# Kernel optimization log

Measured on AMD Instinct MI355X. Metric: run time of the kernel, lower is better.

The kernel has to match this reference:

```python
import jax, jax.numpy as jnp
import numpy as np

H = 8            # kv heads
R = 2            # qhead_ratio -> hq = 16 query heads
D = 128          # head_size
DEG = 2          # power degree
GATE_OFFSET = 6.906768  # ~log(999), gates start near 1


def setup_inputs() -> dict:
    key = jax.random.key(0)
    ks = jax.random.split(key, 7)
    B, T, C = 1, 2048, 2048
    q_dim = H * R * D   # 2048
    kv_dim = H * D      # 1024
    s = 0.02
    return {
        "hidden_states": jax.random.normal(ks[0], (B, T, C), dtype=jnp.float32),
        "Wq": jax.random.normal(ks[1], (C, q_dim), dtype=jnp.float32) * s,
        "Wk": jax.random.normal(ks[2], (C, kv_dim), dtype=jnp.float32) * s,
        "Wv": jax.random.normal(ks[3], (C, kv_dim), dtype=jnp.float32) * s,
        "Wg": jax.random.normal(ks[4], (C, H), dtype=jnp.float32) * s,
        "Wc": jax.random.normal(ks[5], (q_dim, C), dtype=jnp.float32) * s,
        "bc": jnp.zeros((C,), dtype=jnp.float32),
    }


def _power_attention(q, k, v, log_g):
    # q: [B,T,hq,D], k/v: [B,T,H,D], log_g: [B,T,H]
    B, T, hq, d = q.shape
    scale = 1.0 / d ** 0.5
    # GQA: query head i uses kv head i // R (q was viewed as (B,T,H,R,D))
    k = jnp.repeat(k, R, axis=2)            # [B,T,hq,D]
    v = jnp.repeat(v, R, axis=2)            # [B,T,hq,D]
    logG = jnp.cumsum(log_g, axis=1)        # [B,T,H]
    logG = jnp.repeat(logG, R, axis=2)      # [B,T,hq]
    logG = jnp.transpose(logG, (0, 2, 1))   # [B,hq,T]
    qk = jnp.einsum('bthd,bshd->bhts', q, k) * scale   # [B,hq,T,T]
    a = qk ** DEG                                       # even degree -> >= 0
    # gating decay exp(logG_t - logG_s) <= 1 for s <= t
    gate = logG[:, :, :, None] - logG[:, :, None, :]    # [B,hq,T,T]
    causal = jnp.tril(jnp.ones((T, T), dtype=bool))
    a = jnp.where(causal, a * jnp.exp(gate), 0.0)
    norm = jnp.sum(a, axis=-1) + 1e-6                   # [B,hq,T]
    y = jnp.einsum('bhts,bshd->bthd', a, v)             # [B,T,hq,D]
    y = y / jnp.transpose(norm, (0, 2, 1))[..., None]
    return y


def reference(hidden_states, Wq, Wk, Wv, Wg, Wc, bc):
    B, T, C = hidden_states.shape
    q = (hidden_states @ Wq).reshape(B, T, H * R, D)
    k = (hidden_states @ Wk).reshape(B, T, H, D)
    v = (hidden_states @ Wv).reshape(B, T, H, D)
    g = hidden_states @ Wg                              # [B,T,H]
    log_g = jax.nn.log_sigmoid(GATE_OFFSET + g.astype(jnp.float32))
    y = _power_attention(q, k, v, log_g)                # [B,T,hq,D]
    y = y.reshape(B, T, H * R * D)
    return y @ Wc + bc
```

## Files before the change

### kernel.cpp

```cpp
#include <hip/hip_runtime.h>

typedef unsigned short u16;
typedef unsigned int u32;
typedef unsigned long long u64;
typedef __bf16 bf16x8 __attribute__((ext_vector_type(8)));
typedef float f32x4 __attribute__((ext_vector_type(4)));

union FragAB {
  bf16x8 v;
  u16 u[8];
  u32 w[4];
  u64 d2[2];
};

__device__ __forceinline__ u16 f2bf(float f) {
  u32 u = __builtin_bit_cast(u32, f);
  u += 0x7fffu + ((u >> 16) & 1u);
  return (u16)(u >> 16);
}

__device__ __forceinline__ void gload_lds16(const void* g, void* l) {
  __builtin_amdgcn_global_load_lds((__attribute__((address_space(1))) void*)g,
                                   (__attribute__((address_space(3))) void*)l, 16, 0, 0);
}

__device__ __forceinline__ int permcol(int n) {
  int k = n & 31;
  return (n & ~31) | ((k & 12) << 1) | ((k & 16) >> 2) | (k & 3);
}

__global__ __launch_bounds__(256) void conv_perm_kernel(const float* __restrict__ in,
                                                        u16* __restrict__ out, int n4) {
  int i = blockIdx.x * 256 + threadIdx.x;
  if (i >= n4) return;
  float4 v = ((const float4*)in)[i];
  u64 pk = (u64)f2bf(v.x) | ((u64)f2bf(v.y) << 16) | ((u64)f2bf(v.z) << 32) |
           ((u64)f2bf(v.w) << 48);
  int col = (i << 2) & 2047;
  int g = (col >> 2) & 7;
  int ncol = (col & ~31) | ((2 * (g & 3) + (g >> 2)) << 2);
  size_t row = (size_t)(i >> 9);
  *(u64*)&out[row * 2048 + ncol] = pk;
}

__global__ __launch_bounds__(256) void tconv_kernel(const float* __restrict__ in,
                                                    u16* __restrict__ out, int K, int N) {
  __shared__ float tile[32][33];
  int col = threadIdx.x & 31;
  int row0 = threadIdx.x >> 5;
  int kb = blockIdx.y * 32, nb = blockIdx.x * 32;
  int pcol = permcol(col);
#pragma unroll
  for (int i = 0; i < 4; i++) {
    int r = row0 + i * 8;
    tile[r][col] = in[(size_t)(kb + r) * N + nb + col];
  }
  __syncthreads();
#pragma unroll
  for (int i = 0; i < 4; i++) {
    int r = row0 + i * 8;
    out[(size_t)(nb + r) * K + kb + pcol] = f2bf(tile[col][r]);
  }
}

__global__ __launch_bounds__(256) void tconv3_kernel(const float* __restrict__ Wq,
                                                     const float* __restrict__ Wk,
                                                     const float* __restrict__ Wv,
                                                     u16* __restrict__ slab) {
  __shared__ float tile[32][33];
  const int z = blockIdx.z;
  const float* src = (z < 2) ? Wq : (z == 2 ? Wk : Wv);
  const int srcN = (z < 2) ? 2048 : 1024;
  const int colBase = (z == 1) ? 1024 : 0;
  const int dstRowBase = z * 1024;
  int col = threadIdx.x & 31;
  int row0 = threadIdx.x >> 5;
  int kb = blockIdx.y * 32, nb = blockIdx.x * 32;
  int pcol = permcol(col);
#pragma unroll
  for (int i = 0; i < 4; i++) {
    int r = row0 + i * 8;
    tile[r][col] = src[(size_t)(kb + r) * srcN + colBase + nb + col];
  }
  __syncthreads();
#pragma unroll
  for (int i = 0; i < 4; i++) {
    int r = row0 + i * 8;
    slab[(size_t)(dstRowBase + nb + r) * 2048 + kb + pcol] = f2bf(tile[col][r]);
  }
}

__global__ __launch_bounds__(256) void gate_kernel(const float* __restrict__ hs,
                                                   const float* __restrict__ Wg,
                                                   float* __restrict__ lgt) {
  int lane = threadIdx.x & 63, wid = threadIdx.x >> 6;
  int t = blockIdx.x * 4 + wid;
  float acc[8] = {0.f, 0.f, 0.f, 0.f, 0.f, 0.f, 0.f, 0.f};
  for (int c = lane; c < 2048; c += 64) {
    float x = hs[(size_t)t * 2048 + c];
    float4 w0 = *(const float4*)&Wg[c * 8];
    float4 w1 = *(const float4*)&Wg[c * 8 + 4];
    acc[0] += x * w0.x; acc[1] += x * w0.y; acc[2] += x * w0.z; acc[3] += x * w0.w;
    acc[4] += x * w1.x; acc[5] += x * w1.y; acc[6] += x * w1.z; acc[7] += x * w1.w;
  }
#pragma unroll
  for (int h = 0; h < 8; h++) {
    float v = acc[h];
    for (int m = 1; m < 64; m <<= 1) v += __shfl_xor(v, m, 64);
    if (lane == 0) {
      float x = 6.906768f + v;
      lgt[h * 2048 + t] = -log1pf(__expf(-x));
    }
  }
}

__global__ __launch_bounds__(256) void cumsum_kernel(const float* __restrict__ lgt,
                                                     float* __restrict__ logG) {
  int h = blockIdx.x;
  __shared__ float buf[2048];
  for (int i = threadIdx.x; i < 2048; i += 256) buf[i] = lgt[h * 2048 + i];
  __syncthreads();
  for (int off = 1; off < 2048; off <<= 1) {
    float tmp[8];
#pragma unroll
    for (int j = 0; j < 8; j++) {
      int i = threadIdx.x + j * 256;
      tmp[j] = (i >= off) ? buf[i - off] : 0.f;
    }
    __syncthreads();
#pragma unroll
    for (int j = 0; j < 8; j++) {
      int i = threadIdx.x + j * 256;
      buf[i] += tmp[j];
    }
    __syncthreads();
  }
  for (int i = threadIdx.x; i < 2048; i += 256) logG[h * 2048 + i] = buf[i];
}

template <int MODE, int NT>
__global__ __launch_bounds__(512, 4) void gemm_v2(const u16* __restrict__ A,
                                                  const u16* __restrict__ BT,
                                                  void* __restrict__ C0,
                                                  void* __restrict__ C1,
                                                  int permLim) {
  __shared__ __align__(16) u16 As[2 * 128 * 64];
  __shared__ __align__(16) u16 Bs[2 * 128 * 64];
  constexpr int nwg = 16 * NT * (MODE == 2 ? 2 : 1);
  constexpr int cpx = nwg >> 3;
  const int raw = (int)blockIdx.x;
  const int wg = (raw & 7) * cpx + (raw >> 3);
  int bx, by, z;
  if constexpr (MODE == 2) {
    z = wg & 1;
    int t = wg >> 1;
    by = t >> 4;
    bx = t & 15;
  } else {
    z = 0;
    by = wg >> 4;
    bx = wg & 15;
  }
  const int kBeg = (MODE == 2) ? z * 1024 : 0;
  const int kEnd = (MODE == 2) ? kBeg + 1024 : 2048;
  constexpr int N = NT * 128;

  const int tid = threadIdx.x;
  const int lane = tid & 63, wid = tid >> 6;
  const int m0 = bx * 128, n0 = by * 128;
  const int wr = wid >> 2, wc = wid & 3;
  const int l15 = lane & 15, kg = lane >> 4;

  f32x4 acc[4][2];
#pragma unroll
  for (int i = 0; i < 4; i++)
#pragma unroll
    for (int j = 0; j < 2; j++) acc[i][j] = f32x4{0.f, 0.f, 0.f, 0.f};

  const int c0 = (wid * 2) * 64 + lane;
  const int c1 = c0 + 64;
  const int r0 = c0 >> 3, s0u = (c0 & 7) ^ (r0 & 7);
  const int r1 = c1 >> 3, s1u = (c1 & 7) ^ (r1 & 7);
  const u16* Asrc0 = A + (size_t)(m0 + r0) * 2048 + s0u * 8;
  const u16* Asrc1 = A + (size_t)(m0 + r1) * 2048 + s1u * 8;
  const u16* Bsrc0 = BT + (size_t)(n0 + r0) * 2048 + s0u * 8;
  const u16* Bsrc1 = BT + (size_t)(n0 + r1) * 2048 + s1u * 8;

  auto stage = [&](int buf, int k0) {
    u16* Ad = As + buf * 8192 + (wid * 2) * 512;
    u16* Bd = Bs + buf * 8192 + (wid * 2) * 512;
    gload_lds16(Asrc0 + k0, Ad);
    gload_lds16(Asrc1 + k0, Ad + 512);
    gload_lds16(Bsrc0 + k0, Bd);
    gload_lds16(Bsrc1 + k0, Bd + 512);
  };

  stage(0, kBeg);
  __syncthreads();

  int cur = 0;
  for (int k0 = kBeg; k0 < kEnd; k0 += 64) {
    if (k0 + 64 < kEnd) stage(cur ^ 1, k0 + 64);
    const u16* Ab = As + cur * 8192;
    const u16* Bb = Bs + cur * 8192;
#pragma unroll
    for (int ks = 0; ks < 2; ks++) {
      FragAB af[4], bfr[2];
#pragma unroll
      for (int mt = 0; mt < 4; mt++) {
        int row = wr * 64 + mt * 16 + l15;
        af[mt].v = *(const bf16x8*)&Ab[row * 64 + 8 * ((ks * 4 + kg) ^ (row & 7))];
      }
#pragma unroll
      for (int nt = 0; nt < 2; nt++) {
        int row = wc * 32 + nt * 16 + l15;
        bfr[nt].v = *(const bf16x8*)&Bb[row * 64 + 8 * ((ks * 4 + kg) ^ (row & 7))];
      }
#pragma unroll
      for (int mt = 0; mt < 4; mt++)
#pragma unroll
        for (int nt = 0; nt < 2; nt++)
          acc[mt][nt] = __builtin_amdgcn_mfma_f32_16x16x32_bf16(af[mt].v, bfr[nt].v, acc[mt][nt], 0, 0, 0);
    }
    __syncthreads();
    cur ^= 1;
  }

#pragma unroll
  for (int mt = 0; mt < 4; mt++) {
#pragma unroll
    for (int re = 0; re < 4; re++) {
      int m = m0 + wr * 64 + mt * 16 + kg * 4 + re;
#pragma unroll
      for (int nt = 0; nt < 2; nt++) {
        int n = n0 + wc * 32 + nt * 16 + l15;
        float v = acc[mt][nt][re];
        if constexpr (MODE == 2) {
          float* P = z ? (float*)C1 : (float*)C0;
          P[(size_t)m * N + n] = v;
        } else {
          int nw = (n < permLim) ? permcol(n) : n;
          ((u16*)C0)[(size_t)m * N + nw] = f2bf(v);
        }
      }
    }
  }
}

__global__ __launch_bounds__(256, 2) void power_attn(const u16* __restrict__ QKV,
                                                     const float* __restrict__ logG,
                                                     float* __restrict__ y0p,
                                                     float* __restrict__ y1p,
                                                     float* __restrict__ npart) {
  __shared__ __align__(16) u16 Ks[2 * 64 * 128];
  __shared__ __align__(16) u16 Vt[2 * 128 * 64];
  __shared__ float eS[2 * 64];

  const int raw = (int)blockIdx.x;
  const int orig = (raw & 7) * 64 + (raw >> 3);
  const int hq = orig >> 5;
  const int j_ = orig & 31;
  const int half = j_ & 1;
  const int bslot = j_ >> 1;
  const int qa = (bslot + (hq >> 1) * 3) & 15;
  const int qt = (hq & 1) ? (15 - qa) : qa;
  const int hk = hq >> 1;
  const int t0 = qt * 128;

  const int tid = threadIdx.x, lane = tid & 63, wid = tid >> 6;
  const int l15 = lane & 15, kg = lane >> 4;
  const int l7 = l15 & 7;

  const int s4 = tid & 15, dgrp = tid >> 4;
  const int ubase = 4 * (s4 >> 3) + (s4 & 3);
  const int vhb = (s4 >> 2) & 1;

  const u16* Kbase = QKV + 2048 + hk * 128;
  const u16* Vbase = QKV + 3072 + hk * 128 + dgrp * 8;
  const float* lgh = logG + hk * 2048;

  FragAB qf[2][4];
  float celg[2];
  int myT[2];
  const float scale2 = 0.0078125f;
#pragma unroll
  for (int cg = 0; cg < 2; cg++) {
    myT[cg] = t0 + wid * 16 + cg * 64 + l15;
    const u16* qrow = QKV + (size_t)myT[cg] * 4096 + hq * 128;
#pragma unroll
    for (int ks = 0; ks < 4; ks++) qf[cg][ks].v = *(const bf16x8*)(qrow + ks * 32 + kg * 8);
    celg[cg] = scale2 * __expf(lgh[myT[cg]]);
  }

  f32x4 yacc[8][2];
#pragma unroll
  for (int i = 0; i < 8; i++)
#pragma unroll
    for (int c = 0; c < 2; c++) yacc[i][c] = f32x4{0.f, 0.f, 0.f, 0.f};
  float nacc[2] = {0.f, 0.f};

  const int itBeg = half ? (qt + 1) : 0;
  const int itEnd = half ? (2 * qt + 2) : (qt + 1);

  auto stageK = [&](int s0, int bb) {
#pragma unroll
    for (int c = 0; c < 4; c++) {
      int ch = (wid * 4 + c) * 64 + lane;
      int row = ch >> 4, du = ch & 15;
      int su = du ^ (row & 7);
      gload_lds16(Kbase + (size_t)(s0 + row) * 4096 + su * 8, &Ks[bb * 8192 + (wid * 4 + c) * 512]);
    }
  };
  auto loadV = [&](int s0, uint4* vr) {
#pragma unroll
    for (int r = 0; r < 4; r++) vr[r] = *(const uint4*)(Vbase + (size_t)(s0 + 4 * s4 + r) * 4096);
  };
  auto writeV = [&](int bb, const uint4* vr) {
    u16* vd = &Vt[bb * 8192];
    const u32* w0 = (const u32*)&vr[0];
    const u32* w1 = (const u32*)&vr[1];
    const u32* w2 = (const u32*)&vr[2];
    const u32* w3 = (const u32*)&vr[3];
#pragma unroll
    for (int i = 0; i < 8; i++) {
      u32 sel = (i & 1) ? 0x07060302u : 0x05040100u;
      u32 lo = __builtin_amdgcn_perm(w1[i >> 1], w0[i >> 1], sel);
      u32 hi = __builtin_amdgcn_perm(w3[i >> 1], w2[i >> 1], sel);
      int d = dgrp * 8 + i;
      int e = d * 64 + 8 * (ubase ^ i) + 4 * vhb;
      *(u64*)&vd[e] = (u64)lo | ((u64)hi << 32);
    }
  };

  {
    uint4 vr[4];
    stageK(itBeg * 64, 0);
    loadV(itBeg * 64, vr);
    float ee = (tid < 64) ? lgh[itBeg * 64 + tid] : 0.f;
    writeV(0, vr);
    if (tid < 64) eS[tid] = __expf(-ee);
  }
  __syncthreads();

  for (int it = itBeg; it < itEnd; it++) {
    const int cur = (it - itBeg) & 1;
    const int s0 = it * 64;
    const bool hasNext = (it + 1 < itEnd);
    uint4 vr[4];
    float ee = 0.f;
    if (hasNext) {
      stageK(s0 + 64, cur ^ 1);
      loadV(s0 + 64, vr);
      if (tid < 64) ee = lgh[s0 + 64 + tid];
    }

    const u16* kb = &Ks[cur * 8192];
    f32x4 sacc[4][2];
#pragma unroll
    for (int mt = 0; mt < 4; mt++)
#pragma unroll
      for (int cg = 0; cg < 2; cg++) sacc[mt][cg] = f32x4{0.f, 0.f, 0.f, 0.f};
    __builtin_amdgcn_s_setprio(1);
#pragma unroll
    for (int ks = 0; ks < 4; ks++) {
#pragma unroll
      for (int mt = 0; mt < 4; mt++) {
        FragAB af;
        af.v = *(const bf16x8*)&kb[(mt * 16 + l15) * 128 + 8 * ((4 * ks + kg) ^ l7)];
        sacc[mt][0] = __builtin_amdgcn_mfma_f32_16x16x32_bf16(af.v, qf[0][ks].v, sacc[mt][0], 0, 0, 0);
        sacc[mt][1] = __builtin_amdgcn_mfma_f32_16x16x32_bf16(af.v, qf[1][ks].v, sacc[mt][1], 0, 0, 0);
      }
    }
    __builtin_amdgcn_s_setprio(0);

    FragAB pa[2][2];
    const bool need_mask = (it >= 2 * qt);
#pragma unroll
    for (int mt = 0; mt < 4; mt++) {
      f32x4 ev = *(const f32x4*)&eS[cur * 64 + mt * 16 + kg * 4];
#pragma unroll
      for (int cg = 0; cg < 2; cg++) {
        u32 pb[4];
#pragma unroll
        for (int r = 0; r < 4; r++) {
          float x = sacc[mt][cg][r];
          float p = x * x * celg[cg] * ev[r];
          if (need_mask) {
            int s = s0 + mt * 16 + kg * 4 + r;
            p = (s <= myT[cg]) ? p : 0.f;
          }
          nacc[cg] += p;
          pb[r] = __builtin_bit_cast(u32, p) + 0x8000u;
        }
        pa[cg][mt >> 1].w[(mt & 1) * 2 + 0] = __builtin_amdgcn_perm(pb[1], pb[0], 0x07060302u);
        pa[cg][mt >> 1].w[(mt & 1) * 2 + 1] = __builtin_amdgcn_perm(pb[3], pb[2], 0x07060302u);
      }
    }

    const u16* vb = &Vt[cur * 8192];
    const int x0 = 8 * (kg ^ l7);
    __builtin_amdgcn_s_setprio(1);
#pragma unroll
    for (int ksv = 0; ksv < 2; ksv++) {
      const int xo = x0 ^ (ksv * 32);
#pragma unroll
      for (int nt = 0; nt < 8; nt++) {
        FragAB bfv;
        bfv.v = *(const bf16x8*)&vb[(nt * 16 + l15) * 64 + xo];
        yacc[nt][0] = __builtin_amdgcn_mfma_f32_16x16x32_bf16(pa[0][ksv].v, bfv.v, yacc[nt][0], 0, 0, 0);
        yacc[nt][1] = __builtin_amdgcn_mfma_f32_16x16x32_bf16(pa[1][ksv].v, bfv.v, yacc[nt][1], 0, 0, 0);
      }
    }
    __builtin_amdgcn_s_setprio(0);

    if (hasNext) {
      writeV(cur ^ 1, vr);
      if (tid < 64) eS[(cur ^ 1) * 64 + tid] = __expf(-ee);
    }
    __syncthreads();
  }

  float* yp = half ? y1p : y0p;
  float* np = npart + half * (16 * 2048);
#pragma unroll
  for (int cg = 0; cg < 2; cg++) {
    float nf = nacc[cg];
    nf += __shfl_xor(nf, 16, 64);
    nf += __shfl_xor(nf, 32, 64);
    if (lane < 16) np[hq * 2048 + t0 + wid * 16 + cg * 64 + lane] = nf;
#pragma unroll
    for (int re = 0; re < 4; re++) {
      int trow = t0 + wid * 16 + cg * 64 + kg * 4 + re;
      float* yrow = yp + (size_t)trow * 2048 + hq * 128;
#pragma unroll
      for (int nt = 0; nt < 8; nt++) yrow[nt * 16 + l15] = yacc[nt][cg][re];
    }
  }
}

__global__ __launch_bounds__(256) void combine_kernel(const float* __restrict__ y0,
                                                      const float* __restrict__ y1,
                                                      const float* __restrict__ npart,
                                                      u16* __restrict__ yb) {
  int i = blockIdx.x * 256 + threadIdx.x;
  int e0 = i << 2;
  int t = e0 >> 11;
  int hq = (e0 >> 7) & 15;
  float nn = npart[hq * 2048 + t] + npart[32768 + hq * 2048 + t] + 1e-6f;
  float inv = 1.0f / nn;
  float4 a = ((const float4*)y0)[i];
  float4 b = ((const float4*)y1)[i];
  u64 pk = (u64)f2bf((a.x + b.x) * inv) | ((u64)f2bf((a.y + b.y) * inv) << 16) |
           ((u64)f2bf((a.z + b.z) * inv) << 32) | ((u64)f2bf((a.w + b.w) * inv) << 48);
  int col = e0 & 2047;
  int g = (col >> 2) & 7;
  int ncol = (col & ~31) | ((2 * (g & 3) + (g >> 2)) << 2);
  *(u64*)&yb[(size_t)t * 2048 + ncol] = pk;
}

__global__ __launch_bounds__(256) void combine2_kernel(const float* __restrict__ p0,
                                                       float* __restrict__ out,
                                                       const float* __restrict__ bias) {
  int i = blockIdx.x * 256 + threadIdx.x;
  int col = (i << 2) & 2047;
  float4 a = ((const float4*)p0)[i];
  float4 b = ((const float4*)out)[i];
  float4 bb = *(const float4*)&bias[col];
  float4 r;
  r.x = a.x + b.x + bb.x;
  r.y = a.y + b.y + bb.y;
  r.z = a.z + b.z + bb.z;
  r.w = a.w + b.w + bb.w;
  ((float4*)out)[i] = r;
}

extern "C" void kernel_launch(void* const* d_in, const int* in_sizes, int n_in,
                              void* d_out, int out_size, void* d_ws, size_t ws_size,
                              hipStream_t stream) {
  (void)in_sizes; (void)n_in; (void)out_size; (void)ws_size;
  const float* hs = (const float*)d_in[0];
  const float* Wq = (const float*)d_in[1];
  const float* Wk = (const float*)d_in[2];
  const float* Wv = (const float*)d_in[3];
  const float* Wg = (const float*)d_in[4];
  const float* Wc = (const float*)d_in[5];
  const float* bc = (const float*)d_in[6];
  float* out = (float*)d_out;

  char* ws = (char*)d_ws;
  const size_t MB = 1024 * 1024;
  u16* slab   = (u16*)(ws);
  u16* hs_bf  = (u16*)(ws + 16 * MB);
  u16* qkv_bf = (u16*)(ws + 24 * MB);
  float* y0p  = (float*)(ws + 40 * MB);
  float* npart = (float*)(ws + 56 * MB);
  float* lgt  = (float*)(ws + 56 * MB + 262144);
  float* logG = (float*)(ws + 56 * MB + 327680);
  float* y1p = out;
  u16* y_bf = hs_bf;
  u16* WcT = slab;

  conv_perm_kernel<<<4096, 256, 0, stream>>>(hs, hs_bf, 2048 * 2048 / 4);
  tconv3_kernel<<<dim3(32, 64, 4), 256, 0, stream>>>(Wq, Wk, Wv, slab);

  gemm_v2<1, 32><<<512, 512, 0, stream>>>(hs_bf, slab, qkv_bf, nullptr, 3072);

  gate_kernel<<<512, 256, 0, stream>>>(hs, Wg, lgt);
  cumsum_kernel<<<8, 256, 0, stream>>>(lgt, logG);

  tconv_kernel<<<dim3(64, 64), 256, 0, stream>>>(Wc, WcT, 2048, 2048);

  power_attn<<<dim3(512), 256, 0, stream>>>(qkv_bf, logG, y0p, y1p, npart);
  combine_kernel<<<4096, 256, 0, stream>>>(y0p, y1p, npart, y_bf);

  gemm_v2<2, 16><<<512, 512, 0, stream>>>(y_bf, WcT, y0p, out, 0);
  combine2_kernel<<<4096, 256, 0, stream>>>(y0p, out, bc);
}
```

Measured before the change: 164.2 us.

## Fold gating into Q/K projection scales, fuse conv+gate, use bf16 partials

The gate decay exp(logG_t - logG_s) is factored into per-row scales. Q is multiplied by exp(logG/2)*scale and K by exp(-logG/2), applied in the QKV GEMM epilogue, so the attention kernel only squares the scores. The row normalizer is now computed with an MFMA against a ones vector, replacing the scalar accumulation. Other changes: hidden-state conversion is fused with the gate projection, transpose tiles grow to 64x64, and the attention partial outputs are stored as bf16 instead of fp32. Splitting the exponentials this way risks overflow or underflow for long sequences, and bf16 partials lose precision.

Result: slower. 168.6 us (+2.7%).

```diff
diff --git a/kernel.cpp b/kernel.cpp
--- a/kernel.cpp
+++ b/kernel.cpp
@@ -29,79 +29,32 @@
   return (n & ~31) | ((k & 12) << 1) | ((k & 16) >> 2) | (k & 3);
 }
 
-__global__ __launch_bounds__(256) void conv_perm_kernel(const float* __restrict__ in,
-                                                        u16* __restrict__ out, int n4) {
-  int i = blockIdx.x * 256 + threadIdx.x;
-  if (i >= n4) return;
-  float4 v = ((const float4*)in)[i];
-  u64 pk = (u64)f2bf(v.x) | ((u64)f2bf(v.y) << 16) | ((u64)f2bf(v.z) << 32) |
-           ((u64)f2bf(v.w) << 48);
-  int col = (i << 2) & 2047;
-  int g = (col >> 2) & 7;
-  int ncol = (col & ~31) | ((2 * (g & 3) + (g >> 2)) << 2);
-  size_t row = (size_t)(i >> 9);
-  *(u64*)&out[row * 2048 + ncol] = pk;
-}
-
-__global__ __launch_bounds__(256) void tconv_kernel(const float* __restrict__ in,
-                                                    u16* __restrict__ out, int K, int N) {
-  __shared__ float tile[32][33];
-  int col = threadIdx.x & 31;
-  int row0 = threadIdx.x >> 5;
-  int kb = blockIdx.y * 32, nb = blockIdx.x * 32;
-  int pcol = permcol(col);
-#pragma unroll
-  for (int i = 0; i < 4; i++) {
-    int r = row0 + i * 8;
-    tile[r][col] = in[(size_t)(kb + r) * N + nb + col];
-  }
-  __syncthreads();
-#pragma unroll
-  for (int i = 0; i < 4; i++) {
-    int r = row0 + i * 8;
-    out[(size_t)(nb + r) * K + kb + pcol] = f2bf(tile[col][r]);
-  }
-}
-
-__global__ __launch_bounds__(256) void tconv3_kernel(const float* __restrict__ Wq,
-                                                     const float* __restrict__ Wk,
-                                                     const float* __restrict__ Wv,
-                                                     u16* __restrict__ slab) {
-  __shared__ float tile[32][33];
-  const int z = blockIdx.z;
-  const float* src = (z < 2) ? Wq : (z == 2 ? Wk : Wv);
-  const int srcN = (z < 2) ? 2048 : 1024;
-  const int colBase = (z == 1) ? 1024 : 0;
-  const int dstRowBase = z * 1024;
-  int col = threadIdx.x & 31;
-  int row0 = threadIdx.x >> 5;
-  int kb = blockIdx.y * 32, nb = blockIdx.x * 32;
-  int pcol = permcol(col);
-#pragma unroll
-  for (int i = 0; i < 4; i++) {
-    int r = row0 + i * 8;
-    tile[r][col] = src[(size_t)(kb + r) * srcN + colBase + nb + col];
-  }
-  __syncthreads();
-#pragma unroll
-  for (int i = 0; i < 4; i++) {
-    int r = row0 + i * 8;
-    slab[(size_t)(dstRowBase + nb + r) * 2048 + kb + pcol] = f2bf(tile[col][r]);
-  }
-}
-
-__global__ __launch_bounds__(256) void gate_kernel(const float* __restrict__ hs,
-                                                   const float* __restrict__ Wg,
-                                                   float* __restrict__ lgt) {
+__global__ __launch_bounds__(256) void fused_conv_gate(const float* __restrict__ hs,
+                                                       const float* __restrict__ Wg,
+                                                       u16* __restrict__ out,
+                                                       float* __restrict__ lgt) {
   int lane = threadIdx.x & 63, wid = threadIdx.x >> 6;
   int t = blockIdx.x * 4 + wid;
+  const float* row = hs + (size_t)t * 2048;
+  u16* orow = out + (size_t)t * 2048;
   float acc[8] = {0.f, 0.f, 0.f, 0.f, 0.f, 0.f, 0.f, 0.f};
-  for (int c = lane; c < 2048; c += 64) {
-    float x = hs[(size_t)t * 2048 + c];
-    float4 w0 = *(const float4*)&Wg[c * 8];
-    float4 w1 = *(const float4*)&Wg[c * 8 + 4];
-    acc[0] += x * w0.x; acc[1] += x * w0.y; acc[2] += x * w0.z; acc[3] += x * w0.w;
-    acc[4] += x * w1.x; acc[5] += x * w1.y; acc[6] += x * w1.z; acc[7] += x * w1.w;
+#pragma unroll
+  for (int j = 0; j < 8; j++) {
+    int c = j * 256 + lane * 4;
+    float4 v = *(const float4*)&row[c];
+    u64 pk = (u64)f2bf(v.x) | ((u64)f2bf(v.y) << 16) | ((u64)f2bf(v.z) << 32) |
+             ((u64)f2bf(v.w) << 48);
+    int g = (c >> 2) & 7;
+    int ncol = (c & ~31) | ((2 * (g & 3) + (g >> 2)) << 2);
+    *(u64*)&orow[ncol] = pk;
+#pragma unroll
+    for (int e = 0; e < 4; e++) {
+      float x = (e == 0) ? v.x : (e == 1) ? v.y : (e == 2) ? v.z : v.w;
+      float4 w0 = *(const float4*)&Wg[(c + e) * 8];
+      float4 w1 = *(const float4*)&Wg[(c + e) * 8 + 4];
+      acc[0] += x * w0.x; acc[1] += x * w0.y; acc[2] += x * w0.z; acc[3] += x * w0.w;
+      acc[4] += x * w1.x; acc[5] += x * w1.y; acc[6] += x * w1.z; acc[7] += x * w1.w;
+    }
   }
 #pragma unroll
   for (int h = 0; h < 8; h++) {
@@ -114,8 +67,55 @@
   }
 }
 
+__global__ __launch_bounds__(256) void tconv_kernel(const float* __restrict__ in,
+                                                    u16* __restrict__ out, int K, int N) {
+  __shared__ float tile[64][65];
+  int col = threadIdx.x & 63;
+  int r0 = threadIdx.x >> 6;
+  int kb = blockIdx.y * 64, nb = blockIdx.x * 64;
+  int pcol = permcol(col);
+#pragma unroll
+  for (int i = 0; i < 16; i++) {
+    int r = r0 + i * 4;
+    tile[r][col] = in[(size_t)(kb + r) * N + nb + col];
+  }
+  __syncthreads();
+#pragma unroll
+  for (int i = 0; i < 16; i++) {
+    int r = r0 + i * 4;
+    out[(size_t)(nb + r) * K + kb + pcol] = f2bf(tile[col][r]);
+  }
+}
+
+__global__ __launch_bounds__(256) void tconv3_kernel(const float* __restrict__ Wq,
+                                                     const float* __restrict__ Wk,
+                                                     const float* __restrict__ Wv,
+                                                     u16* __restrict__ slab) {
+  const int z = blockIdx.z;
+  if (z > 0 && blockIdx.x >= 16) return;
+  __shared__ float tile[64][65];
+  const float* src = (z == 0) ? Wq : (z == 1 ? Wk : Wv);
+  const int srcN = (z == 0) ? 2048 : 1024;
+  const int dstRowBase = (z == 0) ? 0 : (z == 1 ? 2048 : 3072);
+  int col = threadIdx.x & 63;
+  int r0 = threadIdx.x >> 6;
+  int kb = blockIdx.y * 64, nb = blockIdx.x * 64;
+  int pcol = permcol(col);
+#pragma unroll
+  for (int i = 0; i < 16; i++) {
+    int r = r0 + i * 4;
+    tile[r][col] = src[(size_t)(kb + r) * srcN + nb + col];
+  }
+  __syncthreads();
+#pragma unroll
+  for (int i = 0; i < 16; i++) {
+    int r = r0 + i * 4;
+    slab[(size_t)(dstRowBase + nb + r) * 2048 + kb + pcol] = f2bf(tile[col][r]);
+  }
+}
+
 __global__ __launch_bounds__(256) void cumsum_kernel(const float* __restrict__ lgt,
-                                                     float* __restrict__ logG) {
+                                                     float* __restrict__ scTab) {
   int h = blockIdx.x;
   __shared__ float buf[2048];
   for (int i = threadIdx.x; i < 2048; i += 256) buf[i] = lgt[h * 2048 + i];
@@ -135,7 +135,11 @@
     }
     __syncthreads();
   }
-  for (int i = threadIdx.x; i < 2048; i += 256) logG[h * 2048 + i] = buf[i];
+  for (int i = threadIdx.x; i < 2048; i += 256) {
+    float lg = buf[i];
+    scTab[i * 16 + h] = __expf(0.5f * lg) * 0.08838834764831845f;
+    scTab[i * 16 + 8 + h] = __expf(-0.5f * lg);
+  }
 }
 
 template <int MODE, int NT>
@@ -143,6 +147,7 @@
                                                   const u16* __restrict__ BT,
                                                   void* __restrict__ C0,
                                                   void* __restrict__ C1,
+                                                  const float* __restrict__ scTab,
                                                   int permLim) {
   __shared__ __align__(16) u16 As[2 * 128 * 64];
   __shared__ __align__(16) u16 Bs[2 * 128 * 64];
@@ -239,6 +244,8 @@
           float* P = z ? (float*)C1 : (float*)C0;
           P[(size_t)m * N + n] = v;
         } else {
+          int code = (n < 2048) ? (n >> 8) : ((n < 3072) ? (8 + ((n - 2048) >> 7)) : -1);
+          if (code >= 0) v *= scTab[(size_t)m * 16 + code];
           int nw = (n < permLim) ? permcol(n) : n;
           ((u16*)C0)[(size_t)m * N + nw] = f2bf(v);
         }
@@ -248,13 +255,11 @@
 }
 
 __global__ __launch_bounds__(256, 2) void power_attn(const u16* __restrict__ QKV,
-                                                     const float* __restrict__ logG,
-                                                     float* __restrict__ y0p,
-                                                     float* __restrict__ y1p,
+                                                     u16* __restrict__ y0b,
+                                                     u16* __restrict__ y1b,
                                                      float* __restrict__ npart) {
   __shared__ __align__(16) u16 Ks[2 * 64 * 128];
   __shared__ __align__(16) u16 Vt[2 * 128 * 64];
-  __shared__ float eS[2 * 64];
 
   const int raw = (int)blockIdx.x;
   const int orig = (raw & 7) * 64 + (raw >> 3);
@@ -277,27 +282,27 @@
 
   const u16* Kbase = QKV + 2048 + hk * 128;
   const u16* Vbase = QKV + 3072 + hk * 128 + dgrp * 8;
-  const float* lgh = logG + hk * 2048;
 
   FragAB qf[2][4];
-  float celg[2];
   int myT[2];
-  const float scale2 = 0.0078125f;
 #pragma unroll
   for (int cg = 0; cg < 2; cg++) {
     myT[cg] = t0 + wid * 16 + cg * 64 + l15;
     const u16* qrow = QKV + (size_t)myT[cg] * 4096 + hq * 128;
 #pragma unroll
     for (int ks = 0; ks < 4; ks++) qf[cg][ks].v = *(const bf16x8*)(qrow + ks * 32 + kg * 8);
-    celg[cg] = scale2 * __expf(lgh[myT[cg]]);
-  }
+  }
+
+  FragAB ones;
+#pragma unroll
+  for (int i = 0; i < 8; i++) ones.u[i] = 0x3F80u;
 
   f32x4 yacc[8][2];
 #pragma unroll
   for (int i = 0; i < 8; i++)
 #pragma unroll
     for (int c = 0; c < 2; c++) yacc[i][c] = f32x4{0.f, 0.f, 0.f, 0.f};
-  float nacc[2] = {0.f, 0.f};
+  f32x4 nrm[2] = {f32x4{0.f, 0.f, 0.f, 0.f}, f32x4{0.f, 0.f, 0.f, 0.f}};
 
   const int itBeg = half ? (qt + 1) : 0;
   const int itEnd = half ? (2 * qt + 2) : (qt + 1);
@@ -336,9 +341,7 @@
     uint4 vr[4];
     stageK(itBeg * 64, 0);
     loadV(itBeg * 64, vr);
-    float ee = (tid < 64) ? lgh[itBeg * 64 + tid] : 0.f;
     writeV(0, vr);
-    if (tid < 64) eS[tid] = __expf(-ee);
   }
   __syncthreads();
 
@@ -347,11 +350,9 @@
     const int s0 = it * 64;
     const bool hasNext = (it + 1 < itEnd);
     uint4 vr[4];
-    float ee = 0.f;
     if (hasNext) {
       stageK(s0 + 64, cur ^ 1);
       loadV(s0 + 64, vr);
-      if (tid < 64) ee = lgh[s0 + 64 + tid];
     }
 
     const u16* kb = &Ks[cur * 8192];
@@ -377,19 +378,17 @@
     const bool need_mask = (it >= 2 * qt);
 #pragma unroll
     for (int mt = 0; mt < 4; mt++) {
-      f32x4 ev = *(const f32x4*)&eS[cur * 64 + mt * 16 + kg * 4];
 #pragma unroll
       for (int cg = 0; cg < 2; cg++) {
         u32 pb[4];
 #pragma unroll
         for (int r = 0; r < 4; r++) {
           float x = sacc[mt][cg][r];
-          float p = x * x * celg[cg] * ev[r];
+          float p = x * x;
           if (need_mask) {
             int s = s0 + mt * 16 + kg * 4 + r;
             p = (s <= myT[cg]) ? p : 0.f;
           }
-          nacc[cg] += p;
           pb[r] = __builtin_bit_cast(u32, p) + 0x8000u;
         }
         pa[cg][mt >> 1].w[(mt & 1) * 2 + 0] = __builtin_amdgcn_perm(pb[1], pb[0], 0x07060302u);
@@ -410,48 +409,56 @@
         yacc[nt][0] = __builtin_amdgcn_mfma_f32_16x16x32_bf16(pa[0][ksv].v, bfv.v, yacc[nt][0], 0, 0, 0);
         yacc[nt][1] = __builtin_amdgcn_mfma_f32_16x16x32_bf16(pa[1][ksv].v, bfv.v, yacc[nt][1], 0, 0, 0);
       }
+      nrm[0] = __builtin_amdgcn_mfma_f32_16x16x32_bf16(pa[0][ksv].v, ones.v, nrm[0], 0, 0, 0);
+      nrm[1] = __builtin_amdgcn_mfma_f32_16x16x32_bf16(pa[1][ksv].v, ones.v, nrm[1], 0, 0, 0);
     }
     __builtin_amdgcn_s_setprio(0);
 
-    if (hasNext) {
-      writeV(cur ^ 1, vr);
-      if (tid < 64) eS[(cur ^ 1) * 64 + tid] = __expf(-ee);
-    }
+    if (hasNext) writeV(cur ^ 1, vr);
     __syncthreads();
   }
 
-  float* yp = half ? y1p : y0p;
+  u16* yb = half ? y1b : y0b;
   float* np = npart + half * (16 * 2048);
 #pragma unroll
   for (int cg = 0; cg < 2; cg++) {
-    float nf = nacc[cg];
-    nf += __shfl_xor(nf, 16, 64);
-    nf += __shfl_xor(nf, 32, 64);
-    if (lane < 16) np[hq * 2048 + t0 + wid * 16 + cg * 64 + lane] = nf;
+    if (l15 == 0) {
+#pragma unroll
+      for (int re = 0; re < 4; re++)
+        np[hq * 2048 + t0 + wid * 16 + cg * 64 + kg * 4 + re] = nrm[cg][re];
+    }
 #pragma unroll
     for (int re = 0; re < 4; re++) {
       int trow = t0 + wid * 16 + cg * 64 + kg * 4 + re;
-      float* yrow = yp + (size_t)trow * 2048 + hq * 128;
-#pragma unroll
-      for (int nt = 0; nt < 8; nt++) yrow[nt * 16 + l15] = yacc[nt][cg][re];
-    }
-  }
-}
-
-__global__ __launch_bounds__(256) void combine_kernel(const float* __restrict__ y0,
-                                                      const float* __restrict__ y1,
+      u16* yrow = yb + (size_t)trow * 2048 + hq * 128;
+#pragma unroll
+      for (int nt = 0; nt < 8; nt++) yrow[nt * 16 + l15] = f2bf(yacc[nt][cg][re]);
+    }
+  }
+}
+
+__global__ __launch_bounds__(256) void combine_kernel(const u16* __restrict__ y0b,
+                                                      const u16* __restrict__ y1b,
                                                       const float* __restrict__ npart,
                                                       u16* __restrict__ yb) {
   int i = blockIdx.x * 256 + threadIdx.x;
   int e0 = i << 2;
   int t = e0 >> 11;
   int hq = (e0 >> 7) & 15;
-  float nn = npart[hq * 2048 + t] + npart[32768 + hq * 2048 + t] + 1e-6f;
+  int nidx = hq * 2048 + t;
+  float nn = npart[nidx] + npart[32768 + nidx] + 1e-6f;
   float inv = 1.0f / nn;
-  float4 a = ((const float4*)y0)[i];
-  float4 b = ((const float4*)y1)[i];
-  u64 pk = (u64)f2bf((a.x + b.x) * inv) | ((u64)f2bf((a.y + b.y) * inv) << 16) |
-           ((u64)f2bf((a.z + b.z) * inv) << 32) | ((u64)f2bf((a.w + b.w) * inv) << 48);
+  u64 a0 = *(const u64*)&y0b[e0];
+  u64 a1 = *(const u64*)&y1b[e0];
+  float r[4];
+#pragma unroll
+  for (int j = 0; j < 4; j++) {
+    float v0 = __builtin_bit_cast(float, (u32)((a0 >> (16 * j)) & 0xffffu) << 16);
+    float v1 = __builtin_bit_cast(float, (u32)((a1 >> (16 * j)) & 0xffffu) << 16);
+    r[j] = (v0 + v1) * inv;
+  }
+  u64 pk = (u64)f2bf(r[0]) | ((u64)f2bf(r[1]) << 16) | ((u64)f2bf(r[2]) << 32) |
+           ((u64)f2bf(r[3]) << 48);
   int col = e0 & 2047;
   int g = (col >> 2) & 7;
   int ncol = (col & ~31) | ((2 * (g & 3) + (g >> 2)) << 2);
@@ -491,28 +498,27 @@
   const size_t MB = 1024 * 1024;
   u16* slab   = (u16*)(ws);
   u16* hs_bf  = (u16*)(ws + 16 * MB);
+  u16* y_bf   = (u16*)(ws + 16 * MB);
   u16* qkv_bf = (u16*)(ws + 24 * MB);
+  u16* y0b    = (u16*)(ws + 40 * MB);
   float* y0p  = (float*)(ws + 40 * MB);
-  float* npart = (float*)(ws + 56 * MB);
-  float* lgt  = (float*)(ws + 56 * MB + 262144);
-  float* logG = (float*)(ws + 56 * MB + 327680);
-  float* y1p = out;
-  u16* y_bf = hs_bf;
+  float* lgt   = (float*)(ws + 56 * MB);
+  float* scTab = (float*)(ws + 56 * MB + 65536);
+  float* npart = (float*)(ws + 56 * MB + 65536 + 131072);
+  u16* y1b = (u16*)out;
   u16* WcT = slab;
 
-  conv_perm_kernel<<<4096, 256, 0, stream>>>(hs, hs_bf, 2048 * 2048 / 4);
-  tconv3_kernel<<<dim3(32, 64, 4), 256, 0, stream>>>(Wq, Wk, Wv, slab);
-
-  gemm_v2<1, 32><<<512, 512, 0, stream>>>(hs_bf, slab, qkv_bf, nullptr, 3072);
-
-  gate_kernel<<<512, 256, 0, stream>>>(hs, Wg, lgt);
-  cumsum_kernel<<<8, 256, 0, stream>>>(lgt, logG);
-
-  tconv_kernel<<<dim3(64, 64), 256, 0, stream>>>(Wc, WcT, 2048, 2048);
-
-  power_attn<<<dim3(512), 256, 0, stream>>>(qkv_bf, logG, y0p, y1p, npart);
-  combine_kernel<<<4096, 256, 0, stream>>>(y0p, y1p, npart, y_bf);
-
-  gemm_v2<2, 16><<<512, 512, 0, stream>>>(y_bf, WcT, y0p, out, 0);
+  fused_conv_gate<<<512, 256, 0, stream>>>(hs, Wg, hs_bf, lgt);
+  cumsum_kernel<<<8, 256, 0, stream>>>(lgt, scTab);
+  tconv3_kernel<<<dim3(32, 32, 3), 256, 0, stream>>>(Wq, Wk, Wv, slab);
+
+  gemm_v2<1, 32><<<512, 512, 0, stream>>>(hs_bf, slab, qkv_bf, nullptr, scTab, 3072);
+
+  tconv_kernel<<<dim3(32, 32), 256, 0, stream>>>(Wc, WcT, 2048, 2048);
+
+  power_attn<<<dim3(512), 256, 0, stream>>>(qkv_bf, y0b, y1b, npart);
+  combine_kernel<<<4096, 256, 0, stream>>>(y0b, y1b, npart, y_bf);
+
+  gemm_v2<2, 16><<<512, 512, 0, stream>>>(y_bf, WcT, y0p, out, nullptr, 0);
   combine2_kernel<<<4096, 256, 0, stream>>>(y0p, out, bc);
 }
```
